# Kernel tuning notes

Hardware: AMD Instinct MI355X
Metric: run time of the kernel (lower is better)

The kernel has to match this reference:

```python
import jax, jax.numpy as jnp
import numpy as np

N = 16384        # number of points
NI = 3           # spatial dimension (2 or 3 supported)
BIG = 1e10       # sentinel squared distance for cross-bucket / invalid pairs


def setup_inputs() -> dict:
    key = jax.random.key(0)
    k1, k2 = jax.random.split(key)
    x = jax.random.uniform(k1, (N, NI), dtype=jnp.float32)  # points in [0,1)^NI
    min_t_idx = jax.random.randint(k2, (N,), 0, 4, dtype=jnp.int32)
    return {"x": x, "min_t_idx": min_t_idx, "K": 16, "sz": 5}


def _kde_knn(x, min_t_idx, K, sz):
    n, ni = x.shape
    mask = min_t_idx > 0

    # Spatial hash: cell index per axis (trunc toward zero == torch .long()),
    # flattened row-major with sz as base, offset by min_t_idx * sz**ni.
    y = (x * sz).astype(jnp.int32)                                   # [N, NI]
    weights = jnp.asarray([sz ** (ni - 1 - d) for d in range(ni)], jnp.int32)
    y_f = y @ weights + min_t_idx * (sz ** ni)                        # [N]

    # Pairwise squared distances via gram trick (avoids [N,N,NI] diff tensor).
    sq = jnp.sum(x * x, axis=1)                                       # [N]
    D = sq[:, None] + sq[None, :] - 2.0 * (x @ x.T)                   # [N,N]

    # Block-diagonal ranges in keops == only pairs within the same bucket,
    # restricted to valid (min_t_idx>0) points.  Invalid pairs -> BIG.
    same = (y_f[:, None] == y_f[None, :]) & mask[:, None] & mask[None, :]
    Dm = jnp.where(same, D, BIG)                                      # [N,N]

    # K-th smallest squared distance (self at distance 0 is included,
    # exactly like argKmin over the diagonal ranges).
    kth_sq = -jax.lax.top_k(-Dm, K)[0][:, -1]                         # [N]
    r = jnp.sqrt(jnp.maximum(kth_sq, 0.0))

    # _ball_volume(NI - 1, r)
    dim = ni - 1
    if dim == 1:
        vol = 2.0 * r
    elif dim == 2:
        vol = jnp.pi * r * r
    else:
        vol = (4.0 / 3.0) * jnp.pi * r ** 3

    return jnp.where(mask, vol / (K - 1), 0.0)


def reference(x, min_t_idx, K, sz):
    return _kde_knn(x, min_t_idx, K, sz)
```

## Files before the change

### kernel.cpp

```cpp
#include <hip/hip_runtime.h>


#define KNN 16
#define CAP 2048
#define BIGF 1e10f

__global__ __launch_bounds__(256) void kde_knn_kernel(
    const float* __restrict__ x, const int* __restrict__ mt,
    float* __restrict__ out, int n)
{
    __shared__ float4 mem[CAP];
    __shared__ int cnt;
    const int tid  = threadIdx.x;
    const int lane = tid & 63;
    const int beta = blockIdx.x;
    const int mycell = beta % 125;
    const int mymt   = beta / 125 + 1;

    if (tid == 0) cnt = 0;
    __syncthreads();

    for (int i = tid; i < n; i += 256) {
        int m = mt[i];
        float x0 = x[3 * i + 0];
        float x1 = x[3 * i + 1];
        float x2 = x[3 * i + 2];
        bool member = false;
        if (m > 0) {
            int y0 = (int)(x0 * 5.0f);
            int y1 = (int)(x1 * 5.0f);
            int y2 = (int)(x2 * 5.0f);
            int cell = y0 * 25 + y1 * 5 + y2;
            member = (m == mymt) && (cell == mycell);
        } else {
            if ((unsigned)(i - beta * 44) < 44u) out[i] = 0.0f;
        }
        unsigned long long mask = __ballot(member);
        if (mask) {
            int nfound = __popcll(mask);
            int base = 0;
            if (lane == 0) base = atomicAdd(&cnt, nfound);
            base = __shfl(base, 0);
            if (member) {
                int prefix = __popcll(mask & ((1ull << lane) - 1ull));
                int pos = base + prefix;
                if (pos < CAP)
                    mem[pos] = make_float4(x0, x1, x2, __int_as_float(i));
            }
        }
    }
    __syncthreads();

    int c = cnt;
    if (c > CAP) c = CAP;
    for (int t = tid; t < c; t += 256) {
        float4 p = mem[t];
        float best[KNN];
#pragma unroll
        for (int k = 0; k < KNN; ++k) best[k] = BIGF;
        float curmax = BIGF;
        int maxpos = 0;

        for (int u = 0; u < c; ++u) {
            float4 q = mem[u];
            float dx = p.x - q.x;
            float dy = p.y - q.y;
            float dz = p.z - q.z;
            float d2 = dx * dx + dy * dy + dz * dz;
            if (d2 < curmax) {
#pragma unroll
                for (int k = 0; k < KNN; ++k)
                    if (k == maxpos) best[k] = d2;
                curmax = best[0]; maxpos = 0;
#pragma unroll
                for (int k = 1; k < KNN; ++k)
                    if (best[k] > curmax) { curmax = best[k]; maxpos = k; }
            }
        }

        int i = __float_as_int(p.w);
        float r = sqrtf(fmaxf(curmax, 0.0f));
        float vol = 3.14159265358979323846f * r * r;
        out[i] = vol / 15.0f;
    }
}

extern "C" void kernel_launch(void* const* d_in, const int* in_sizes, int n_in,
                              void* d_out, int out_size, void* d_ws, size_t ws_size,
                              hipStream_t stream) {
    const float* x  = (const float*)d_in[0];
    const int*   mt = (const int*)d_in[1];
    float* out = (float*)d_out;
    int n = in_sizes[1];

    kde_knn_kernel<<<375, 256, 0, stream>>>(x, mt, out, n);
}
```

Measured before the change: 98.66 us.

## Vectorize bucket scan with float4 loads, 1024-thread blocks, smaller shared cap

The scan over all points now reads coordinates and bucket indices as float4/int4 vectors, four points per thread, and blocks grow from 256 to 1024 threads. Shared-memory capacity per bucket drops from 2048 to 256 entries. This is meant to cut the memory-bound scan time, since every block reads the whole input. The risks are that buckets over 256 points get truncated (expected size is about 33, so this is unlikely), that the code assumes n is a multiple of 4 with aligned pointers, and that the compute phase leaves most of the 1024 threads idle.

```diff
diff --git a/kernel.cpp b/kernel.cpp
--- a/kernel.cpp
+++ b/kernel.cpp
@@ -2,10 +2,10 @@
 
 
 #define KNN 16
-#define CAP 2048
+#define CAP 256
 #define BIGF 1e10f
 
-__global__ __launch_bounds__(256) void kde_knn_kernel(
+__global__ __launch_bounds__(1024) void kde_knn_kernel(
     const float* __restrict__ x, const int* __restrict__ mt,
     float* __restrict__ out, int n)
 {
@@ -20,32 +20,46 @@
     if (tid == 0) cnt = 0;
     __syncthreads();
 
-    for (int i = tid; i < n; i += 256) {
-        int m = mt[i];
-        float x0 = x[3 * i + 0];
-        float x1 = x[3 * i + 1];
-        float x2 = x[3 * i + 2];
-        bool member = false;
-        if (m > 0) {
-            int y0 = (int)(x0 * 5.0f);
-            int y1 = (int)(x1 * 5.0f);
-            int y2 = (int)(x2 * 5.0f);
-            int cell = y0 * 25 + y1 * 5 + y2;
-            member = (m == mymt) && (cell == mycell);
-        } else {
-            if ((unsigned)(i - beta * 44) < 44u) out[i] = 0.0f;
-        }
-        unsigned long long mask = __ballot(member);
-        if (mask) {
-            int nfound = __popcll(mask);
-            int base = 0;
-            if (lane == 0) base = atomicAdd(&cnt, nfound);
-            base = __shfl(base, 0);
-            if (member) {
-                int prefix = __popcll(mask & ((1ull << lane) - 1ull));
-                int pos = base + prefix;
-                if (pos < CAP)
-                    mem[pos] = make_float4(x0, x1, x2, __int_as_float(i));
+    const float4* __restrict__ xv = (const float4*)x;
+    const int4*   __restrict__ mv = (const int4*)mt;
+
+    for (int base_i = 0; base_i < n; base_i += 4 * 1024) {
+        int k  = base_i / 4 + tid;
+        int i0 = 4 * k;
+        if (i0 < n) {
+            int4   m4 = mv[k];
+            float4 a  = xv[3 * k + 0];
+            float4 b  = xv[3 * k + 1];
+            float4 c4 = xv[3 * k + 2];
+            float px[4] = { a.x,  a.w,  b.z,  c4.y };
+            float py[4] = { a.y,  b.x,  b.w,  c4.z };
+            float pz[4] = { a.z,  b.y,  c4.x, c4.w };
+            int   mm[4] = { m4.x, m4.y, m4.z, m4.w };
+#pragma unroll
+            for (int s = 0; s < 4; ++s) {
+                int i = i0 + s;
+                bool member = false;
+                if (mm[s] > 0) {
+                    int y0 = (int)(px[s] * 5.0f);
+                    int y1 = (int)(py[s] * 5.0f);
+                    int y2 = (int)(pz[s] * 5.0f);
+                    member = (mm[s] == mymt) &&
+                             (y0 * 25 + y1 * 5 + y2 == mycell);
+                } else if ((unsigned)(i - beta * 44) < 44u) {
+                    out[i] = 0.0f;
+                }
+                unsigned long long mask = __ballot(member);
+                if (mask) {
+                    int bs = 0;
+                    if (lane == 0) bs = atomicAdd(&cnt, __popcll(mask));
+                    bs = __shfl(bs, 0);
+                    if (member) {
+                        int pos = bs + __popcll(mask & ((1ull << lane) - 1ull));
+                        if (pos < CAP)
+                            mem[pos] = make_float4(px[s], py[s], pz[s],
+                                                   __int_as_float(i));
+                    }
+                }
             }
         }
     }
@@ -53,11 +67,11 @@
 
     int c = cnt;
     if (c > CAP) c = CAP;
-    for (int t = tid; t < c; t += 256) {
+    for (int t = tid; t < c; t += 1024) {
         float4 p = mem[t];
         float best[KNN];
 #pragma unroll
-        for (int k = 0; k < KNN; ++k) best[k] = BIGF;
+        for (int k2 = 0; k2 < KNN; ++k2) best[k2] = BIGF;
         float curmax = BIGF;
         int maxpos = 0;
 
@@ -69,12 +83,12 @@
             float d2 = dx * dx + dy * dy + dz * dz;
             if (d2 < curmax) {
 #pragma unroll
-                for (int k = 0; k < KNN; ++k)
-                    if (k == maxpos) best[k] = d2;
+                for (int k2 = 0; k2 < KNN; ++k2)
+                    if (k2 == maxpos) best[k2] = d2;
                 curmax = best[0]; maxpos = 0;
 #pragma unroll
-                for (int k = 1; k < KNN; ++k)
-                    if (best[k] > curmax) { curmax = best[k]; maxpos = k; }
+                for (int k2 = 1; k2 < KNN; ++k2)
+                    if (best[k2] > curmax) { curmax = best[k2]; maxpos = k2; }
             }
         }
 
@@ -93,5 +107,5 @@
     float* out = (float*)d_out;
     int n = in_sizes[1];
 
-    kde_knn_kernel<<<375, 256, 0, stream>>>(x, mt, out, n);
+    kde_knn_kernel<<<375, 1024, 0, stream>>>(x, mt, out, n);
 }
```

Result: faster. 82.01 us (-16.9%).
